# Kernel optimization log

Measured on AMD Instinct MI355X. Metric: run time of the kernel, lower is better.

The kernel has to match this reference:

```python
import jax
import jax.numpy as jnp
import numpy as np

N_NODES = 4096
N_EDGES = 65536
D_FEAT = 64


def setup_inputs() -> dict:
    key = jax.random.key(0)
    k1, k2, k3, k4 = jax.random.split(key, 4)
    x = jax.random.normal(k1, (N_NODES, D_FEAT), dtype=jnp.float32)
    edge_index = jax.random.randint(k2, (2, N_EDGES), 0, N_NODES, dtype=jnp.int32)
    batch = jnp.zeros((N_NODES,), dtype=jnp.int32)
    # GraphConv(in_channels, 1): lin_rel (with bias) on aggregated neighbors, lin_root on self
    w_rel = jax.random.normal(k3, (D_FEAT, 1), dtype=jnp.float32) * 0.1
    w_root = jax.random.normal(k4, (D_FEAT, 1), dtype=jnp.float32) * 0.1
    b = jnp.zeros((1,), dtype=jnp.float32)
    return {"x": x, "edge_index": edge_index, "batch": batch,
            "w_rel": w_rel, "w_root": w_root, "b": b}


def _merge_stars(x, src0, dst0, score):
    """Faithful sequential greedy star contraction (priority order by score desc)."""
    N = x.shape[0]
    order = jnp.argsort(-score)  # descending, ties like argsort

    def step(carry, node):
        xc, src, dst, remaining, center = carry
        active = remaining[node]
        # dests = set of targets of edges whose (current, rewritten) source == node,
        # minus already-chosen center nodes
        dest_edge = src == node                                  # [E]
        dest_node = jnp.zeros(N, bool).at[dst].max(dest_edge)    # node-level set
        dest_node = dest_node & ~center
        # torch does sum over list(dests)+[node]: node counted again (even on self-loop)
        combine = jnp.einsum('n,nd->d', dest_node.astype(xc.dtype), xc) + xc[node]
        D = dest_node.at[node].set(True)                         # dests U {node}
        x2 = xc.at[node].set(combine)
        src2 = jnp.where(D[src], node, src)                      # np.isin rewrite
        dst2 = jnp.where(D[dst], node, dst)
        rem2 = remaining & ~dest_node
        cen2 = center.at[node].set(True)
        carry2 = (jnp.where(active, x2, xc),
                  jnp.where(active, src2, src),
                  jnp.where(active, dst2, dst),
                  jnp.where(active, rem2, remaining),
                  jnp.where(active, cen2, center))
        return carry2, None

    init = (x, src0, dst0, jnp.ones(N, bool), jnp.zeros(N, bool))
    (x_final, _, _, remaining, _), _ = jax.lax.scan(step, init, order)
    return x_final, remaining


def reference(x, edge_index, batch, w_rel, w_root, b):
    N, d = x.shape
    src0, dst0 = edge_index[0], edge_index[1]
    # GraphConv score: W_rel * sum_{j->i} x_j + b + W_root * x_i ; dropout p=0; tanh
    agg = jax.ops.segment_sum(x[src0], dst0, num_segments=N)     # [N, d]
    score = jnp.tanh((agg @ w_rel + x @ w_root + b).reshape(-1)) # [N]

    x_final, remaining = _merge_stars(x, src0, dst0, score)

    # perm = sorted(nodes_remaining); outputs padded to static size N (sentinel -1)
    perm = jnp.nonzero(remaining, size=N, fill_value=N)[0]
    x_pooled = jnp.take(x_final, perm, axis=0, mode='fill', fill_value=0.0)
    kept = perm < N
    batch_pooled = jnp.where(kept, jnp.take(batch, jnp.minimum(perm, N - 1)), -1)
    # filter_adj on the ORIGINAL edge_index: keep edges with both endpoints kept,
    # relabel nodes to their rank among kept nodes; invalid edges -> -1
    relabel = jnp.cumsum(remaining.astype(jnp.int32)) - 1
    valid = remaining[src0] & remaining[dst0]
    new_src = jnp.where(valid, relabel[src0], -1)
    new_dst = jnp.where(valid, relabel[dst0], -1)
    new_edge_index = jnp.stack([new_src, new_dst])
    perm_out = jnp.where(kept, perm, -1)
    return x_pooled, new_edge_index, batch_pooled, perm_out
```

## Files before the change

kernel.cpp:

```cpp
#include <hip/hip_runtime.h>

#define NN 4096
#define NE 65536
#define ND 64
#define BCAP 44

__global__ void kA_pre(const float* __restrict__ x, const int* __restrict__ ei,
                       const float* __restrict__ wrel, const float* __restrict__ wroot,
                       double* __restrict__ srel, double* __restrict__ sroot,
                       int* __restrict__ gcnt, unsigned short* __restrict__ gbuf,
                       float* __restrict__ out) {
    int gtid = blockIdx.x * blockDim.x + threadIdx.x;
    int lane = threadIdx.x & 63;

    float4* o4 = (float4*)out;
    o4[gtid] = make_float4(0.f, 0.f, 0.f, 0.f);

    int gwave = gtid >> 6;
    for (int node = gwave; node < NN; node += 1024) {
        double xv = (double)x[node * ND + lane];
        double pr = xv * (double)wrel[lane];
        double po = xv * (double)wroot[lane];
        for (int off = 32; off > 0; off >>= 1) {
            pr += __shfl_down(pr, off);
            po += __shfl_down(po, off);
        }
        if (lane == 0) { srel[node] = pr; sroot[node] = po; }
    }

    int s = ei[gtid], d = ei[NE + gtid];
    int pos = atomicAdd(&gcnt[d], 1);
    if (pos < BCAP) gbuf[d * BCAP + pos] = (unsigned short)s;
}

__global__ void __launch_bounds__(1024) kB_contract(
        const double* __restrict__ srel, const double* __restrict__ sroot,
        const float* __restrict__ bptr, const int* __restrict__ gcnt,
        const unsigned short* __restrict__ gbuf,
        int* __restrict__ map_g, int* __restrict__ rem_g, int* __restrict__ relab_g,
        int* __restrict__ perm_a, int* __restrict__ nkeep_g) {
    __shared__ __align__(16) char buf[163840];
    unsigned short* incsr = (unsigned short*)buf;
    char* aux = buf + 131072;
    double* srel_lds = (double*)aux;
    volatile unsigned long long* skey = (volatile unsigned long long*)aux;
    int* wt = (int*)(aux + 20544);
    int tid = threadIdx.x, lane = tid & 63, wv = tid >> 6;

    int4 d4 = ((const int4*)gcnt)[tid];
    int t0 = min(d4.x, BCAP), t1 = min(d4.y, BCAP);
    int t2 = min(d4.z, BCAP), t3 = min(d4.w, BCAP);
    int tot = t0 + t1 + t2 + t3;
    int inc = tot;
    for (int off = 1; off < 64; off <<= 1) {
        int v = __shfl_up(inc, off);
        if (lane >= off) inc += v;
    }
    if (lane == 63) wt[wv] = inc;
    __syncthreads();
    if (wv == 0 && lane < 16) {
        int v = wt[lane];
        for (int off = 1; off < 16; off <<= 1) {
            int u2 = __shfl_up(v, off);
            if (lane >= off) v += u2;
        }
        wt[lane] = v;
    }
    __syncthreads();
    int waveoff = (wv > 0) ? wt[wv - 1] : 0;
    int excl = waveoff + inc - tot;
    int rs4[4], re4[4];
    rs4[0] = excl; rs4[1] = excl + t0; rs4[2] = excl + t0 + t1; rs4[3] = excl + t0 + t1 + t2;
    re4[0] = rs4[1]; re4[1] = rs4[2]; re4[2] = rs4[3]; re4[3] = rs4[3] + t3;
    __syncthreads();

    for (int t = 0; t < 4; ++t) {
        int v = 4 * tid + t;
        const unsigned short* gp = gbuf + v * BCAP;
        int base = rs4[t], dg = re4[t] - rs4[t];
        int j = 0;
        for (; j + 4 <= dg; j += 4) {
            ushort4 q = *(const ushort4*)(gp + j);
            incsr[base + j] = q.x; incsr[base + j + 1] = q.y;
            incsr[base + j + 2] = q.z; incsr[base + j + 3] = q.w;
        }
        for (; j < dg; ++j) incsr[base + j] = gp[j];
    }

    {
        double2* sl2 = (double2*)aux;
        const double2* sg2 = (const double2*)srel;
        for (int i = tid; i < NN / 2; i += 1024) sl2[i] = sg2[i];
    }
    __syncthreads();

    double bv = (double)bptr[0];
    unsigned long long base4[4];
    for (int t = 0; t < 4; ++t) {
        int v = 4 * tid + t;
        double s = 0.0;
        for (int e = rs4[t]; e < re4[t]; ++e) s += srel_lds[(int)incsr[e]];
        double arg = s + sroot[v] + bv;
        float sc = tanhf((float)arg);
        unsigned m = __float_as_uint(sc);
        m = (m & 0x80000000u) ? ~m : (m | 0x80000000u);
        base4[t] = ((unsigned long long)(~m) << 14) | ((unsigned long long)v << 2);
    }
    __syncthreads();

    for (int t = 0; t < 4; ++t) skey[4 * tid + t] = base4[t];
    __syncthreads();

    unsigned long long pk4[4], minC4[4];
    unsigned resolved = 0, centerm = 0, selfm = 0;
    for (int t = 0; t < 4; ++t) {
        int v = 4 * tid + t;
        unsigned long long pkv = base4[t] >> 2;
        pk4[t] = pkv; minC4[t] = ~0ULL;
        int w = rs4[t];
        for (int e = rs4[t]; e < re4[t]; ++e) {
            int u = (int)incsr[e];
            if (u == v) { selfm |= 1u << t; continue; }
            unsigned long long ku = skey[u] >> 2;
            if (ku < pkv) incsr[w++] = (unsigned short)u;
        }
        re4[t] = w;
        if (w == rs4[t]) {
            map_g[v] = v;
            skey[v] = base4[t] | 1ULL;
            centerm |= 1u << t; resolved |= 1u << t;
        }
    }

    int guard = 0;
    while (resolved != 0xFu && guard < 1000000) {
        ++guard;
        bool prog = false;
        for (int t = 0; t < 4; ++t) {
            if (resolved & (1u << t)) continue;
            int v = 4 * tid + t;
            int lo = rs4[t], hi = re4[t];
            unsigned long long minU = ~0ULL, mC = minC4[t];
            int w = lo;
            for (int e = lo; e < hi; ++e) {
                int u = (int)incsr[e];
                unsigned long long sk = skey[u];
                int st = (int)(sk & 3ULL);
                unsigned long long ku = sk >> 2;
                if (st == 0) { incsr[w++] = (unsigned short)u; if (ku < minU) minU = ku; }
                else if (st == 1) { if (ku < mC) mC = ku; }
            }
            if (w != hi) prog = true;
            re4[t] = w; minC4[t] = mC;
            if (mC < minU) {
                map_g[v] = (int)(mC & 0xFFFULL);
                skey[v] = (pk4[t] << 2) | 2ULL;
                resolved |= 1u << t; prog = true;
            } else if (w == lo) {
                map_g[v] = v;
                skey[v] = (pk4[t] << 2) | 1ULL;
                centerm |= 1u << t; resolved |= 1u << t; prog = true;
            }
        }
        if (!prog) __builtin_amdgcn_s_sleep(1);
    }
    __syncthreads();

    int remb[4], cnt4 = 0;
    for (int t = 0; t < 4; ++t) {
        remb[t] = ((centerm >> t) & 1) && !((selfm >> t) & 1);
        cnt4 += remb[t];
    }
    int inc2 = cnt4;
    for (int off = 1; off < 64; off <<= 1) {
        int v = __shfl_up(inc2, off);
        if (lane >= off) inc2 += v;
    }
    if (lane == 63) wt[wv] = inc2;
    __syncthreads();
    if (wv == 0 && lane < 16) {
        int v = wt[lane];
        for (int off = 1; off < 16; off <<= 1) {
            int u2 = __shfl_up(v, off);
            if (lane >= off) v += u2;
        }
        wt[lane] = v;
    }
    __syncthreads();
    int woff2 = (wv > 0) ? wt[wv - 1] : 0;
    int run = woff2 + inc2 - cnt4;
    for (int t = 0; t < 4; ++t) {
        int v = 4 * tid + t;
        relab_g[v] = run;
        if (remb[t]) { perm_a[run] = v; ++run; }
        rem_g[v] = remb[t];
    }
    if (tid == 1023) nkeep_g[0] = run;
}

__global__ void kC_outputs(const float* __restrict__ x, const int* __restrict__ map_g,
                           const int* __restrict__ rem_g, const int* __restrict__ relab_g,
                           const int* __restrict__ perm_a, const int* __restrict__ ei,
                           const int* __restrict__ batch, const int* __restrict__ nkeep_g,
                           float* __restrict__ out) {
    int idx = blockIdx.x * blockDim.x + threadIdx.x;
    if (idx < NN * ND) {
        int n = idx >> 6, d = idx & 63;
        int m = map_g[n];
        if (rem_g[m]) atomicAdd(&out[relab_g[m] * ND + d], x[idx]);
    } else if (idx < NN * ND + 2 * NE) {
        int e = idx - NN * ND;
        int row = e >> 16;
        int ee = e & (NE - 1);
        int s = ei[ee], t = ei[NE + ee];
        bool valid = (rem_g[s] != 0) && (rem_g[t] != 0);
        int endp = (row == 0) ? s : t;
        out[idx] = valid ? (float)relab_g[endp] : -1.0f;
    } else if (idx < NN * ND + 2 * NE + NN) {
        int r = idx - (NN * ND + 2 * NE);
        int nk = nkeep_g[0];
        out[idx] = (r < nk) ? (float)batch[perm_a[r]] : -1.0f;
    } else if (idx < NN * ND + 2 * NE + 2 * NN) {
        int r = idx - (NN * ND + 2 * NE + NN);
        int nk = nkeep_g[0];
        out[idx] = (r < nk) ? (float)perm_a[r] : -1.0f;
    }
}

extern "C" void kernel_launch(void* const* d_in, const int* in_sizes, int n_in,
                              void* d_out, int out_size, void* d_ws, size_t ws_size,
                              hipStream_t stream) {
    const float* x     = (const float*)d_in[0];
    const int*   ei    = (const int*)d_in[1];
    const int*   batch = (const int*)d_in[2];
    const float* wrel  = (const float*)d_in[3];
    const float* wroot = (const float*)d_in[4];
    const float* b     = (const float*)d_in[5];

    char* ws = (char*)d_ws;
    double*         srel  = (double*)(ws + 0);
    double*         sroot = (double*)(ws + 32768);
    int*            map_g = (int*)(ws + 65536);
    int*            rem_g = (int*)(ws + 81920);
    int*            relab = (int*)(ws + 98304);
    int*            perma = (int*)(ws + 114688);
    int*            nkeep = (int*)(ws + 131072);
    int*            gcnt  = (int*)(ws + 131200);
    unsigned short* gbuf  = (unsigned short*)(ws + 147584);

    float* out = (float*)d_out;

    hipMemsetAsync(gcnt, 0, NN * sizeof(int), stream);
    kA_pre<<<256, 256, 0, stream>>>(x, ei, wrel, wroot, srel, sroot, gcnt, gbuf, out);
    kB_contract<<<1, 1024, 0, stream>>>(srel, sroot, b, gcnt, gbuf, map_g, rem_g,
                                        relab, perma, nkeep);
    int total_out = NN * ND + 2 * NE + 2 * NN;
    kC_outputs<<<(total_out + 255) / 256, 256, 0, stream>>>(x, map_g, rem_g, relab,
                                                            perma, ei, batch, nkeep, out);
}
```

Measured before the change: 171.1 us.

## Replace polling greedy contraction with counter-driven push-based resolution

Builds an outgoing (source-indexed) adjacency bucket alongside the incoming one. The greedy star contraction now keeps, per node, a count of unresolved higher-priority in-neighbours. Once a node resolves it pushes its key via atomicMin to lower-priority out-neighbours and decrements their counters, so nodes no longer rescan their in-lists on every polling pass. This trades repeated LDS scans for extra atomics, a second scatter and scan in the pre-pass, and more LDS pressure.

Result: slower. 308.3 us (+80.1%).

```diff
diff --git a/kernel.cpp b/kernel.cpp
--- a/kernel.cpp
+++ b/kernel.cpp
@@ -8,7 +8,8 @@
 __global__ void kA_pre(const float* __restrict__ x, const int* __restrict__ ei,
                        const float* __restrict__ wrel, const float* __restrict__ wroot,
                        double* __restrict__ srel, double* __restrict__ sroot,
-                       int* __restrict__ gcnt, unsigned short* __restrict__ gbuf,
+                       int* __restrict__ gcnt_d, int* __restrict__ gcnt_s,
+                       unsigned short* __restrict__ gbuf_d, unsigned short* __restrict__ gbuf_s,
                        float* __restrict__ out) {
     int gtid = blockIdx.x * blockDim.x + threadIdx.x;
     int lane = threadIdx.x & 63;
@@ -29,25 +30,32 @@
     }
 
     int s = ei[gtid], d = ei[NE + gtid];
-    int pos = atomicAdd(&gcnt[d], 1);
-    if (pos < BCAP) gbuf[d * BCAP + pos] = (unsigned short)s;
+    int pd = atomicAdd(&gcnt_d[d], 1);
+    if (pd < BCAP) gbuf_d[d * BCAP + pd] = (unsigned short)s;
+    int ps = atomicAdd(&gcnt_s[s], 1);
+    if (ps < BCAP) gbuf_s[s * BCAP + ps] = (unsigned short)d;
 }
 
 __global__ void __launch_bounds__(1024) kB_contract(
         const double* __restrict__ srel, const double* __restrict__ sroot,
-        const float* __restrict__ bptr, const int* __restrict__ gcnt,
-        const unsigned short* __restrict__ gbuf,
+        const float* __restrict__ bptr, const int* __restrict__ gcnt_d,
+        const unsigned short* __restrict__ gbuf_d, const int* __restrict__ gcnt_s,
+        const unsigned short* __restrict__ gbuf_s,
         int* __restrict__ map_g, int* __restrict__ rem_g, int* __restrict__ relab_g,
         int* __restrict__ perm_a, int* __restrict__ nkeep_g) {
     __shared__ __align__(16) char buf[163840];
     unsigned short* incsr = (unsigned short*)buf;
+    int* cntv = (int*)buf;
+    unsigned long long* best = (unsigned long long*)(buf + 16384);
+    unsigned short* outl = (unsigned short*)(buf + 49152);
+    int* wt2 = (int*)(buf + 131008);
     char* aux = buf + 131072;
     double* srel_lds = (double*)aux;
     volatile unsigned long long* skey = (volatile unsigned long long*)aux;
     int* wt = (int*)(aux + 20544);
     int tid = threadIdx.x, lane = tid & 63, wv = tid >> 6;
 
-    int4 d4 = ((const int4*)gcnt)[tid];
+    int4 d4 = ((const int4*)gcnt_d)[tid];
     int t0 = min(d4.x, BCAP), t1 = min(d4.y, BCAP);
     int t2 = min(d4.z, BCAP), t3 = min(d4.w, BCAP);
     int tot = t0 + t1 + t2 + t3;
@@ -76,7 +84,7 @@
 
     for (int t = 0; t < 4; ++t) {
         int v = 4 * tid + t;
-        const unsigned short* gp = gbuf + v * BCAP;
+        const unsigned short* gp = gbuf_d + v * BCAP;
         int base = rs4[t], dg = re4[t] - rs4[t];
         int j = 0;
         for (; j + 4 <= dg; j += 4) {
@@ -95,7 +103,7 @@
     __syncthreads();
 
     double bv = (double)bptr[0];
-    unsigned long long base4[4];
+    unsigned long long pk4[4];
     for (int t = 0; t < 4; ++t) {
         int v = 4 * tid + t;
         double s = 0.0;
@@ -104,79 +112,120 @@
         float sc = tanhf((float)arg);
         unsigned m = __float_as_uint(sc);
         m = (m & 0x80000000u) ? ~m : (m | 0x80000000u);
-        base4[t] = ((unsigned long long)(~m) << 14) | ((unsigned long long)v << 2);
-    }
-    __syncthreads();
-
-    for (int t = 0; t < 4; ++t) skey[4 * tid + t] = base4[t];
-    __syncthreads();
-
-    unsigned long long pk4[4], minC4[4];
-    unsigned resolved = 0, centerm = 0, selfm = 0;
-    for (int t = 0; t < 4; ++t) {
-        int v = 4 * tid + t;
-        unsigned long long pkv = base4[t] >> 2;
-        pk4[t] = pkv; minC4[t] = ~0ULL;
-        int w = rs4[t];
+        pk4[t] = ((unsigned long long)(~m) << 12) | (unsigned long long)v;
+    }
+    __syncthreads();
+
+    for (int t = 0; t < 4; ++t) skey[4 * tid + t] = pk4[t] << 2;
+    __syncthreads();
+
+    int cnt4[4];
+    unsigned centerm = 0, selfm = 0;
+    for (int t = 0; t < 4; ++t) {
+        int v = 4 * tid + t;
+        int c = 0;
         for (int e = rs4[t]; e < re4[t]; ++e) {
             int u = (int)incsr[e];
             if (u == v) { selfm |= 1u << t; continue; }
-            unsigned long long ku = skey[u] >> 2;
-            if (ku < pkv) incsr[w++] = (unsigned short)u;
-        }
-        re4[t] = w;
-        if (w == rs4[t]) {
-            map_g[v] = v;
-            skey[v] = base4[t] | 1ULL;
-            centerm |= 1u << t; resolved |= 1u << t;
-        }
-    }
-
+            if ((skey[u] >> 2) < pk4[t]) ++c;
+        }
+        cnt4[t] = c;
+    }
+    __syncthreads();
+
+    int m4[4];
+    for (int t = 0; t < 4; ++t) {
+        int v = 4 * tid + t;
+        int od = min(gcnt_s[v], BCAP);
+        const unsigned short* gp = gbuf_s + v * BCAP;
+        int m = 0;
+        for (int j = 0; j < od; ++j) {
+            int w = (int)gp[j];
+            if (w == v) continue;
+            if (pk4[t] < (skey[w] >> 2)) ++m;
+        }
+        m4[t] = m;
+    }
+    int tot2 = m4[0] + m4[1] + m4[2] + m4[3];
+    int inc2 = tot2;
+    for (int off = 1; off < 64; off <<= 1) {
+        int v = __shfl_up(inc2, off);
+        if (lane >= off) inc2 += v;
+    }
+    if (lane == 63) wt2[wv] = inc2;
+    __syncthreads();
+    if (wv == 0 && lane < 16) {
+        int v = wt2[lane];
+        for (int off = 1; off < 16; off <<= 1) {
+            int u2 = __shfl_up(v, off);
+            if (lane >= off) v += u2;
+        }
+        wt2[lane] = v;
+    }
+    __syncthreads();
+    int woff = (wv > 0) ? wt2[wv - 1] : 0;
+    int obase = woff + inc2 - tot2;
+    int os4[4];
+    os4[0] = obase; os4[1] = obase + m4[0];
+    os4[2] = os4[1] + m4[1]; os4[3] = os4[2] + m4[2];
+
+    for (int t = 0; t < 4; ++t) {
+        int v = 4 * tid + t;
+        int od = min(gcnt_s[v], BCAP);
+        const unsigned short* gp = gbuf_s + v * BCAP;
+        int c = os4[t];
+        for (int j = 0; j < od; ++j) {
+            int w = (int)gp[j];
+            if (w == v) continue;
+            if (pk4[t] < (skey[w] >> 2)) outl[c++] = (unsigned short)w;
+        }
+    }
+    for (int t = 0; t < 4; ++t) {
+        int v = 4 * tid + t;
+        cntv[v] = cnt4[t];
+        best[v] = ~0ULL;
+    }
+    __syncthreads();
+
+    unsigned resolved = 0;
     int guard = 0;
-    while (resolved != 0xFu && guard < 1000000) {
+    while (resolved != 0xFu && guard < 4000000) {
         ++guard;
         bool prog = false;
         for (int t = 0; t < 4; ++t) {
             if (resolved & (1u << t)) continue;
             int v = 4 * tid + t;
-            int lo = rs4[t], hi = re4[t];
-            unsigned long long minU = ~0ULL, mC = minC4[t];
-            int w = lo;
-            for (int e = lo; e < hi; ++e) {
-                int u = (int)incsr[e];
-                unsigned long long sk = skey[u];
-                int st = (int)(sk & 3ULL);
-                unsigned long long ku = sk >> 2;
-                if (st == 0) { incsr[w++] = (unsigned short)u; if (ku < minU) minU = ku; }
-                else if (st == 1) { if (ku < mC) mC = ku; }
+            if (*(volatile int*)(cntv + v) > 0) continue;
+            unsigned long long bvv = *(volatile unsigned long long*)(best + v);
+            int s0 = os4[t], s1 = os4[t] + m4[t];
+            if (bvv == ~0ULL) {
+                map_g[v] = v;
+                centerm |= 1u << t;
+                unsigned long long kq = pk4[t];
+                for (int j = s0; j < s1; ++j) atomicMin(&best[(int)outl[j]], kq);
+                __threadfence_block();
+            } else {
+                map_g[v] = (int)(bvv & 0xFFFULL);
             }
-            if (w != hi) prog = true;
-            re4[t] = w; minC4[t] = mC;
-            if (mC < minU) {
-                map_g[v] = (int)(mC & 0xFFFULL);
-                skey[v] = (pk4[t] << 2) | 2ULL;
-                resolved |= 1u << t; prog = true;
-            } else if (w == lo) {
-                map_g[v] = v;
-                skey[v] = (pk4[t] << 2) | 1ULL;
-                centerm |= 1u << t; resolved |= 1u << t; prog = true;
-            }
+            for (int j = s0; j < s1; ++j) atomicSub(&cntv[(int)outl[j]], 1);
+            resolved |= 1u << t;
+            prog = true;
         }
         if (!prog) __builtin_amdgcn_s_sleep(1);
     }
     __syncthreads();
 
-    int remb[4], cnt4 = 0;
+    int remb[4], cnt4b = 0;
     for (int t = 0; t < 4; ++t) {
         remb[t] = ((centerm >> t) & 1) && !((selfm >> t) & 1);
-        cnt4 += remb[t];
-    }
-    int inc2 = cnt4;
+        cnt4b += remb[t];
+    }
+    int inc3 = cnt4b;
     for (int off = 1; off < 64; off <<= 1) {
-        int v = __shfl_up(inc2, off);
-        if (lane >= off) inc2 += v;
-    }
-    if (lane == 63) wt[wv] = inc2;
+        int v = __shfl_up(inc3, off);
+        if (lane >= off) inc3 += v;
+    }
+    if (lane == 63) wt[wv] = inc3;
     __syncthreads();
     if (wv == 0 && lane < 16) {
         int v = wt[lane];
@@ -188,7 +237,7 @@
     }
     __syncthreads();
     int woff2 = (wv > 0) ? wt[wv - 1] : 0;
-    int run = woff2 + inc2 - cnt4;
+    int run = woff2 + inc3 - cnt4b;
     for (int t = 0; t < 4; ++t) {
         int v = 4 * tid + t;
         relab_g[v] = run;
@@ -238,22 +287,25 @@
     const float* b     = (const float*)d_in[5];
 
     char* ws = (char*)d_ws;
-    double*         srel  = (double*)(ws + 0);
-    double*         sroot = (double*)(ws + 32768);
-    int*            map_g = (int*)(ws + 65536);
-    int*            rem_g = (int*)(ws + 81920);
-    int*            relab = (int*)(ws + 98304);
-    int*            perma = (int*)(ws + 114688);
-    int*            nkeep = (int*)(ws + 131072);
-    int*            gcnt  = (int*)(ws + 131200);
-    unsigned short* gbuf  = (unsigned short*)(ws + 147584);
+    double*         srel   = (double*)(ws + 0);
+    double*         sroot  = (double*)(ws + 32768);
+    int*            map_g  = (int*)(ws + 65536);
+    int*            rem_g  = (int*)(ws + 81920);
+    int*            relab  = (int*)(ws + 98304);
+    int*            perma  = (int*)(ws + 114688);
+    int*            nkeep  = (int*)(ws + 131072);
+    int*            gcnt_d = (int*)(ws + 131200);
+    int*            gcnt_s = (int*)(ws + 147584);
+    unsigned short* gbuf_d = (unsigned short*)(ws + 163968);
+    unsigned short* gbuf_s = (unsigned short*)(ws + 524416);
 
     float* out = (float*)d_out;
 
-    hipMemsetAsync(gcnt, 0, NN * sizeof(int), stream);
-    kA_pre<<<256, 256, 0, stream>>>(x, ei, wrel, wroot, srel, sroot, gcnt, gbuf, out);
-    kB_contract<<<1, 1024, 0, stream>>>(srel, sroot, b, gcnt, gbuf, map_g, rem_g,
-                                        relab, perma, nkeep);
+    hipMemsetAsync(gcnt_d, 0, 32768, stream);
+    kA_pre<<<256, 256, 0, stream>>>(x, ei, wrel, wroot, srel, sroot, gcnt_d, gcnt_s,
+                                    gbuf_d, gbuf_s, out);
+    kB_contract<<<1, 1024, 0, stream>>>(srel, sroot, b, gcnt_d, gbuf_d, gcnt_s, gbuf_s,
+                                        map_g, rem_g, relab, perma, nkeep);
     int total_out = NN * ND + 2 * NE + 2 * NN;
     kC_outputs<<<(total_out + 255) / 256, 256, 0, stream>>>(x, map_g, rem_g, relab,
                                                             perma, ei, batch, nkeep, out);
```

## Sort higher-priority in-neighbors and walk them in order instead of rescanning

Applied to the files above, without the earlier changes.

For nodes with at most 16 higher-priority in-neighbors, the keys are bitonic-sorted in registers. Each node then watches only the highest-priority unresolved neighbor, advancing a pointer past neighbors that became absorbed rather than rescanning the whole list every iteration. Nodes with more neighbors keep the old full-rescan path. The idle sleep now fires only every fourth idle iteration. This cuts per-iteration LDS traffic in the spin loop, at the cost of extra register pressure from the 16-element key array and the sorting network.

Result: slower. 203.5 us (+18.9%).

```diff
diff --git a/kernel.cpp b/kernel.cpp
--- a/kernel.cpp
+++ b/kernel.cpp
@@ -29,8 +29,8 @@
     }
 
     int s = ei[gtid], d = ei[NE + gtid];
-    int pos = atomicAdd(&gcnt[d], 1);
-    if (pos < BCAP) gbuf[d * BCAP + pos] = (unsigned short)s;
+    int pd = atomicAdd(&gcnt[d], 1);
+    if (pd < BCAP) gbuf[d * BCAP + pd] = (unsigned short)s;
 }
 
 __global__ void __launch_bounds__(1024) kB_contract(
@@ -95,7 +95,7 @@
     __syncthreads();
 
     double bv = (double)bptr[0];
-    unsigned long long base4[4];
+    unsigned long long pk4[4];
     for (int t = 0; t < 4; ++t) {
         int v = 4 * tid + t;
         double s = 0.0;
@@ -104,79 +104,143 @@
         float sc = tanhf((float)arg);
         unsigned m = __float_as_uint(sc);
         m = (m & 0x80000000u) ? ~m : (m | 0x80000000u);
-        base4[t] = ((unsigned long long)(~m) << 14) | ((unsigned long long)v << 2);
-    }
-    __syncthreads();
-
-    for (int t = 0; t < 4; ++t) skey[4 * tid + t] = base4[t];
-    __syncthreads();
-
-    unsigned long long pk4[4], minC4[4];
-    unsigned resolved = 0, centerm = 0, selfm = 0;
+        pk4[t] = ((unsigned long long)(~m) << 12) | (unsigned long long)v;
+    }
+    __syncthreads();
+
+    for (int t = 0; t < 4; ++t) skey[4 * tid + t] = pk4[t] << 2;
+    __syncthreads();
+
+    unsigned long long minC4[4];
+    int ptr4[4], uh4[4];
+    unsigned resolved = 0, centerm = 0, selfm = 0, walkm = 0;
     for (int t = 0; t < 4; ++t) {
         int v = 4 * tid + t;
-        unsigned long long pkv = base4[t] >> 2;
-        pk4[t] = pkv; minC4[t] = ~0ULL;
+        unsigned long long pkv = pk4[t];
+        minC4[t] = ~0ULL;
         int w = rs4[t];
         for (int e = rs4[t]; e < re4[t]; ++e) {
             int u = (int)incsr[e];
             if (u == v) { selfm |= 1u << t; continue; }
-            unsigned long long ku = skey[u] >> 2;
-            if (ku < pkv) incsr[w++] = (unsigned short)u;
+            if ((skey[u] >> 2) < pkv) incsr[w++] = (unsigned short)u;
         }
         re4[t] = w;
-        if (w == rs4[t]) {
+        int m = w - rs4[t];
+        if (m == 0) {
             map_g[v] = v;
-            skey[v] = base4[t] | 1ULL;
+            skey[v] = (pkv << 2) | 1ULL;
             centerm |= 1u << t; resolved |= 1u << t;
-        }
-    }
-
-    int guard = 0;
+        } else if (m <= 16) {
+            walkm |= 1u << t;
+            unsigned long long kk[16];
+            int base = rs4[t];
+#pragma unroll
+            for (int j = 0; j < 16; ++j)
+                kk[j] = (j < m) ? (skey[(int)incsr[base + j]] & ~3ULL) : ~0ULL;
+#pragma unroll
+            for (int k2 = 2; k2 <= 16; k2 <<= 1) {
+#pragma unroll
+                for (int j2 = k2 >> 1; j2 > 0; j2 >>= 1) {
+#pragma unroll
+                    for (int i2 = 0; i2 < 16; ++i2) {
+                        int l2 = i2 ^ j2;
+                        if (l2 > i2) {
+                            bool up = ((i2 & k2) == 0);
+                            if ((kk[i2] > kk[l2]) == up) {
+                                unsigned long long tmp = kk[i2];
+                                kk[i2] = kk[l2]; kk[l2] = tmp;
+                            }
+                        }
+                    }
+                }
+            }
+#pragma unroll
+            for (int j = 0; j < 16; ++j)
+                if (j < m) incsr[base + j] = (unsigned short)((kk[j] >> 2) & 0xFFFULL);
+            ptr4[t] = base;
+            uh4[t] = (int)((kk[0] >> 2) & 0xFFFULL);
+        }
+    }
+
+    int guard = 0, idle = 0;
     while (resolved != 0xFu && guard < 1000000) {
         ++guard;
         bool prog = false;
         for (int t = 0; t < 4; ++t) {
             if (resolved & (1u << t)) continue;
             int v = 4 * tid + t;
-            int lo = rs4[t], hi = re4[t];
-            unsigned long long minU = ~0ULL, mC = minC4[t];
-            int w = lo;
-            for (int e = lo; e < hi; ++e) {
-                int u = (int)incsr[e];
-                unsigned long long sk = skey[u];
+            if (walkm & (1u << t)) {
+                unsigned long long sk = skey[uh4[t]];
                 int st = (int)(sk & 3ULL);
-                unsigned long long ku = sk >> 2;
-                if (st == 0) { incsr[w++] = (unsigned short)u; if (ku < minU) minU = ku; }
-                else if (st == 1) { if (ku < mC) mC = ku; }
+                if (st == 1) {
+                    map_g[v] = (int)((sk >> 2) & 0xFFFULL);
+                    skey[v] = (pk4[t] << 2) | 2ULL;
+                    resolved |= 1u << t; prog = true;
+                } else if (st == 2) {
+                    int p = ptr4[t] + 1, end = re4[t];
+                    int u = -1; unsigned long long s2 = 0;
+                    while (p < end) {
+                        u = (int)incsr[p];
+                        s2 = skey[u];
+                        if ((s2 & 3ULL) == 2ULL) { ++p; continue; }
+                        break;
+                    }
+                    if (p >= end) {
+                        map_g[v] = v;
+                        skey[v] = (pk4[t] << 2) | 1ULL;
+                        centerm |= 1u << t; resolved |= 1u << t;
+                    } else {
+                        ptr4[t] = p; uh4[t] = u;
+                        if ((s2 & 3ULL) == 1ULL) {
+                            map_g[v] = (int)((s2 >> 2) & 0xFFFULL);
+                            skey[v] = (pk4[t] << 2) | 2ULL;
+                            resolved |= 1u << t;
+                        }
+                    }
+                    prog = true;
+                }
+            } else {
+                int lo = rs4[t], hi = re4[t];
+                unsigned long long minU = ~0ULL, mC = minC4[t];
+                int w = lo;
+                for (int e = lo; e < hi; ++e) {
+                    int u = (int)incsr[e];
+                    unsigned long long sk = skey[u];
+                    int st = (int)(sk & 3ULL);
+                    unsigned long long ku = sk >> 2;
+                    if (st == 0) { incsr[w++] = (unsigned short)u; if (ku < minU) minU = ku; }
+                    else if (st == 1) { if (ku < mC) mC = ku; }
+                }
+                if (w != hi) prog = true;
+                re4[t] = w; minC4[t] = mC;
+                if (mC < minU) {
+                    map_g[v] = (int)(mC & 0xFFFULL);
+                    skey[v] = (pk4[t] << 2) | 2ULL;
+                    resolved |= 1u << t; prog = true;
+                } else if (w == lo) {
+                    map_g[v] = v;
+                    skey[v] = (pk4[t] << 2) | 1ULL;
+                    centerm |= 1u << t; resolved |= 1u << t; prog = true;
+                }
             }
-            if (w != hi) prog = true;
-            re4[t] = w; minC4[t] = mC;
-            if (mC < minU) {
-                map_g[v] = (int)(mC & 0xFFFULL);
-                skey[v] = (pk4[t] << 2) | 2ULL;
-                resolved |= 1u << t; prog = true;
-            } else if (w == lo) {
-                map_g[v] = v;
-                skey[v] = (pk4[t] << 2) | 1ULL;
-                centerm |= 1u << t; resolved |= 1u << t; prog = true;
-            }
-        }
-        if (!prog) __builtin_amdgcn_s_sleep(1);
-    }
-    __syncthreads();
-
-    int remb[4], cnt4 = 0;
+        }
+        if (!prog) {
+            if (((++idle) & 3) == 0) __builtin_amdgcn_s_sleep(1);
+        } else idle = 0;
+    }
+    __syncthreads();
+
+    int remb[4], cnt4b = 0;
     for (int t = 0; t < 4; ++t) {
         remb[t] = ((centerm >> t) & 1) && !((selfm >> t) & 1);
-        cnt4 += remb[t];
-    }
-    int inc2 = cnt4;
+        cnt4b += remb[t];
+    }
+    int inc3 = cnt4b;
     for (int off = 1; off < 64; off <<= 1) {
-        int v = __shfl_up(inc2, off);
-        if (lane >= off) inc2 += v;
-    }
-    if (lane == 63) wt[wv] = inc2;
+        int v = __shfl_up(inc3, off);
+        if (lane >= off) inc3 += v;
+    }
+    if (lane == 63) wt[wv] = inc3;
     __syncthreads();
     if (wv == 0 && lane < 16) {
         int v = wt[lane];
@@ -188,7 +252,7 @@
     }
     __syncthreads();
     int woff2 = (wv > 0) ? wt[wv - 1] : 0;
-    int run = woff2 + inc2 - cnt4;
+    int run = woff2 + inc3 - cnt4b;
     for (int t = 0; t < 4; ++t) {
         int v = 4 * tid + t;
         relab_g[v] = run;
```
